# Optimization experiments

Hardware: AMD Instinct MI355X
Metric: run time of the kernel (lower is better)

## Reference

```python
import jax, jax.numpy as jnp
import numpy as np

B, T_ENC, T_DEC = 32, 256, 256
ENC, HID, ATT, CCH, K = 512, 1024, 128, 32, 31
OUT, PRE = 80, 256
ZONEOUT = 0.1
P_DROP = 0.5
PAD = (K - 1) // 2


def setup_inputs() -> dict:
    key = jax.random.key(0)
    ks = jax.random.split(key, 20)
    def n(k, shape, s=0.02):
        return jax.random.normal(k, shape, dtype=jnp.float32) * s
    inp = {}
    inp["encoder_outs"] = jax.random.normal(ks[0], (B, T_ENC, ENC), dtype=jnp.float32)
    inp["decoder_targets"] = jax.random.normal(ks[1], (B, T_DEC, OUT), dtype=jnp.float32)
    keep = 1.0 - P_DROP
    # pre-sampled inverted-dropout masks for the 2 prenet layers at every step
    inp["prenet_masks"] = jax.random.bernoulli(ks[2], keep, (T_DEC, 2, B, PRE)).astype(jnp.float32) / keep
    inp["in_lens"] = jax.random.randint(ks[3], (B,), T_ENC // 2, T_ENC + 1, dtype=jnp.int32)
    # location-sensitive attention params
    inp["V_w"] = n(ks[4], (ATT, ENC)); inp["V_b"] = jnp.zeros((ATT,), jnp.float32)
    inp["W_w"] = n(ks[5], (ATT, HID))
    inp["U_w"] = n(ks[6], (ATT, CCH))
    inp["F_w"] = n(ks[7], (CCH, 1, K))
    inp["w_w"] = n(ks[8], (1, ATT)); inp["w_b"] = jnp.zeros((1,), jnp.float32)
    # prenet
    inp["pre_w0"] = n(ks[9], (PRE, OUT)); inp["pre_b0"] = jnp.zeros((PRE,), jnp.float32)
    inp["pre_w1"] = n(ks[10], (PRE, PRE)); inp["pre_b1"] = jnp.zeros((PRE,), jnp.float32)
    # stacked LSTM cells (zoneout wrappers)
    inp["l0_wih"] = n(ks[11], (4 * HID, ENC + PRE)); inp["l0_whh"] = n(ks[12], (4 * HID, HID))
    inp["l0_bih"] = jnp.zeros((4 * HID,), jnp.float32); inp["l0_bhh"] = jnp.zeros((4 * HID,), jnp.float32)
    inp["l1_wih"] = n(ks[13], (4 * HID, HID)); inp["l1_whh"] = n(ks[14], (4 * HID, HID))
    inp["l1_bih"] = jnp.zeros((4 * HID,), jnp.float32); inp["l1_bhh"] = jnp.zeros((4 * HID,), jnp.float32)
    # output projections
    inp["feat_w"] = n(ks[15], (OUT, ENC + HID))
    inp["prob_w"] = n(ks[16], (1, ENC + HID)); inp["prob_b"] = jnp.zeros((1,), jnp.float32)
    return inp


def _lstm_cell(x, h, c, wih, whh, bih, bhh):
    g = x @ wih.T + bih + h @ whh.T + bhh
    i, f, gg, o = jnp.split(g, 4, axis=1)  # torch LSTMCell gate order
    c2 = jax.nn.sigmoid(f) * c + jax.nn.sigmoid(i) * jnp.tanh(gg)
    h2 = jax.nn.sigmoid(o) * jnp.tanh(c2)
    return h2, c2


def _decode(encoder_outs, decoder_targets, prenet_masks, in_lens,
            V_w, V_b, W_w, U_w, F_w, w_w, w_b,
            pre_w0, pre_b0, pre_w1, pre_b1,
            l0_wih, l0_whh, l0_bih, l0_bhh,
            l1_wih, l1_whh, l1_bih, l1_bhh,
            feat_w, prob_w, prob_b):
    b = encoder_outs.shape[0]
    pad_mask = jnp.arange(T_ENC)[None, :] >= in_lens[:, None]       # [B,T_enc] True = pad
    att_uniform = (~pad_mask).astype(jnp.float32) / in_lens[:, None].astype(jnp.float32)
    processed_memory = encoder_outs @ V_w.T + V_b                   # [B,T_enc,ATT]
    neg = jnp.float32(-1e9)

    # teacher forcing: prev_out at step 0 is the go-frame, then target[t-1]
    targets_prev = jnp.concatenate(
        [jnp.zeros((b, 1, OUT), jnp.float32), decoder_targets[:, :-1]], axis=1)
    xs = (jnp.swapaxes(targets_prev, 0, 1), prenet_masks[:, 0], prenet_masks[:, 1],
          jnp.arange(T_DEC))

    def step(carry, x):
        h0, c0, h1, c1, cum = carry
        prev_out, m0, m1, t = x
        # location-sensitive attention (prev_att_w = None at t=0 -> uniform over valid)
        att_prev = jnp.where(t == 0, att_uniform, cum)              # [B,T_enc]
        f = jax.lax.conv_general_dilated(
            att_prev[:, None, :], F_w, (1,), [(PAD, PAD)],
            dimension_numbers=("NCH", "OIH", "NCH"))                # [B,CCH,T_enc]
        f = jnp.swapaxes(f, 1, 2)                                   # [B,T_enc,CCH]
        erg = jnp.tanh(processed_memory + (h0 @ W_w.T)[:, None, :] + f @ U_w.T)
        erg = (erg @ w_w.T + w_b)[..., 0]                           # [B,T_enc]
        erg = jnp.where(pad_mask, neg, erg)
        aw = jax.nn.softmax(erg, axis=1)
        att_c = jnp.einsum("bt,bte->be", aw, encoder_outs)          # [B,ENC]
        # prenet (dropout always on, via pre-sampled masks)
        p = jax.nn.relu(prev_out @ pre_w0.T + pre_b0) * m0
        p = jax.nn.relu(p @ pre_w1.T + pre_b1) * m1
        xin = jnp.concatenate([att_c, p], axis=1)
        # zoneout LSTM stack (eval-mode zoneout: convex mix of prev/new states)
        h0n, c0n = _lstm_cell(xin, h0, c0, l0_wih, l0_whh, l0_bih, l0_bhh)
        h0 = ZONEOUT * h0 + (1.0 - ZONEOUT) * h0n
        c0 = ZONEOUT * c0 + (1.0 - ZONEOUT) * c0n
        h1n, c1n = _lstm_cell(h0, h1, c1, l1_wih, l1_whh, l1_bih, l1_bhh)
        h1 = ZONEOUT * h1 + (1.0 - ZONEOUT) * h1n
        c1 = ZONEOUT * c1 + (1.0 - ZONEOUT) * c1n
        hcs = jnp.concatenate([h1, att_c], axis=1)                  # [B,HID+ENC]
        out = hcs @ feat_w.T                                        # [B,OUT] (no bias)
        logit = hcs @ prob_w.T + prob_b                             # [B,1]
        return (h0, c0, h1, c1, cum + aw), (out, logit, aw)

    z = jnp.zeros((b, HID), jnp.float32)
    carry0 = (z, z, z, z, jnp.zeros((b, T_ENC), jnp.float32))
    _, (outs, logits, att_ws) = jax.lax.scan(step, carry0, xs)
    outs = jnp.transpose(outs, (1, 2, 0))      # [B,OUT,T_dec]
    logits = logits[..., 0].T                  # [B,T_dec]
    att_ws = jnp.swapaxes(att_ws, 0, 1)        # [B,T_dec,T_enc]
    return outs, logits, att_ws


def reference(encoder_outs, decoder_targets, prenet_masks, in_lens,
              V_w, V_b, W_w, U_w, F_w, w_w, w_b,
              pre_w0, pre_b0, pre_w1, pre_b1,
              l0_wih, l0_whh, l0_bih, l0_bhh,
              l1_wih, l1_whh, l1_bih, l1_bhh,
              feat_w, prob_w, prob_b):
    return _decode(encoder_outs, decoder_targets, prenet_masks, in_lens,
                   V_w, V_b, W_w, U_w, F_w, w_w, w_b,
                   pre_w0, pre_b0, pre_w1, pre_b1,
                   l0_wih, l0_whh, l0_bih, l0_bhh,
                   l1_wih, l1_whh, l1_bih, l1_bhh,
                   feat_w, prob_w, prob_b)
```

## Files before the change

### kernel.cpp

```cpp
#include <hip/hip_runtime.h>

typedef _Float16 half2_t __attribute__((ext_vector_type(2)));
typedef unsigned uint_t;

#define B_    32
#define TE_   256
#define TD_   256
#define ENC_  512
#define HID_  1024
#define ATT_  128
#define OUT_  80
#define PRE_  256

#define LOG_OFF  655360u
#define ATTW_OFF 663552u

#define OFF_PM    0u
#define OFF_P1H   1048576u
#define OFF_M     2097152u
#define OFF_WWHT  2101248u
#define OFF_ENCH  2166784u
#define OFF_W0P   4263936u
#define OFF_W1P   7933952u
#define OFF_XC0   12128256u
#define OFF_XC1   12173312u
#define OFF_C0    12206080u
#define OFF_C1    12238848u
#define OFF_CUM   12271616u
#define OFF_ATTC  12279808u
#define OFF_END   12328960u

__device__ __forceinline__ float rcp_f(float x){ return __builtin_amdgcn_rcpf(x); }
__device__ __forceinline__ float sigm(float x){ return rcp_f(1.0f + __expf(-x)); }
__device__ __forceinline__ float tanh_f(float x){ float e = __expf(2.0f*x); return 1.0f - 2.0f*rcp_f(e+1.0f); }

__device__ __forceinline__ uint_t packh2(float a, float b){
  half2_t h; h[0] = (_Float16)a; h[1] = (_Float16)b;
  return __builtin_bit_cast(uint_t, h);
}
__device__ __forceinline__ float dot2f(uint_t w, uint_t x, float c){
#if __has_builtin(__builtin_amdgcn_fdot2)
  return __builtin_amdgcn_fdot2(__builtin_bit_cast(half2_t, w),
                                __builtin_bit_cast(half2_t, x), c, false);
#else
  half2_t a = __builtin_bit_cast(half2_t, w), b = __builtin_bit_cast(half2_t, x);
  return c + (float)a[0]*(float)b[0] + (float)a[1]*(float)b[1];
#endif
}


__global__ void k_init(float* __restrict__ ws){
  unsigned n = OFF_END - OFF_XC0;
  for (unsigned i = blockIdx.x*blockDim.x + threadIdx.x; i < n; i += gridDim.x*blockDim.x)
    ws[OFF_XC0 + i] = 0.f;
}

__global__ void k_precm(const float* __restrict__ Uw, const float* __restrict__ Fw,
                        float* __restrict__ ws){
  float* M = ws + OFF_M;
  for (int idx = threadIdx.x; idx < 128*31; idx += blockDim.x){
    int a = idx / 31, k = idx % 31;
    float s = 0.f;
    for (int c = 0; c < 32; c++) s += Uw[a*32+c]*Fw[c*31+k];
    M[idx] = s;
  }
}

__global__ void k_cvtww(const float* __restrict__ Ww, float* __restrict__ ws){
  uint_t* WT = (uint_t*)(ws + OFF_WWHT);
  int p = blockIdx.x;
  for (int a = threadIdx.x; a < 128; a += blockDim.x)
    WT[p*128 + a] = packh2(Ww[a*1024 + 2*p], Ww[a*1024 + 2*p + 1]);
}

__global__ void k_packenc(const float* __restrict__ enc, float* __restrict__ ws){
  uint_t* ENCH = (uint_t*)(ws + OFF_ENCH);
  size_t row = blockIdx.x;
  for (int j = threadIdx.x; j < 256; j += blockDim.x)
    ENCH[row*256 + j] = packh2(enc[row*512 + 2*j], enc[row*512 + 2*j + 1]);
}

__global__ void k_packw0(const float* __restrict__ wih, const float* __restrict__ whh,
                         float* __restrict__ ws){
  uint_t* W = (uint_t*)(ws + OFF_W0P);
  size_t r = blockIdx.x;
  for (int p = threadIdx.x; p < 896; p += blockDim.x){
    int k = 2*p;
    const float* src = (k < 768) ? (wih + r*768 + k) : (whh + r*1024 + (k-768));
    W[r*896 + p] = packh2(src[0], src[1]);
  }
}

__global__ void k_packw1(const float* __restrict__ wih, const float* __restrict__ whh,
                         float* __restrict__ ws){
  uint_t* W = (uint_t*)(ws + OFF_W1P);
  size_t r = blockIdx.x;
  for (int p = threadIdx.x; p < 1024; p += blockDim.x){
    int k = 2*p;
    const float* src = (k < 1024) ? (wih + r*1024 + k) : (whh + r*1024 + (k-1024));
    W[r*1024 + p] = packh2(src[0], src[1]);
  }
}

__global__ __launch_bounds__(256) void k_pm(const float* __restrict__ enc,
    const float* __restrict__ Vw, const float* __restrict__ Vb, float* __restrict__ ws){
  float* pm = ws + OFF_PM;
  int b  = blockIdx.x >> 2;
  int s0 = (blockIdx.x & 3) << 6;
  int a  = threadIdx.x & 127;
  int sh = threadIdx.x >> 7;
  __shared__ float Vl[128*65];
  __shared__ float El[64*64];
  float acc[32];
  #pragma unroll
  for (int i=0;i<32;i++) acc[i]=0.f;
  for (int kc=0; kc<ENC_; kc+=64){
    for (int i=threadIdx.x; i<128*64; i+=256){
      int aa = i>>6, kk = i&63;
      Vl[aa*65+kk] = Vw[aa*ENC_ + kc + kk];
    }
    for (int i=threadIdx.x; i<64*64; i+=256){
      int ss = i>>6, kk = i&63;
      El[i] = enc[(size_t)(b*TE_ + s0 + ss)*ENC_ + kc + kk];
    }
    __syncthreads();
    for (int k=0;k<64;k++){
      float va = Vl[a*65+k];
      const float* er = &El[(sh*32)*64 + k];
      #pragma unroll
      for (int s=0;s<32;s++) acc[s] += va * er[s*64];
    }
    __syncthreads();
  }
  float bb = Vb[a];
  for (int s=0;s<32;s++)
    pm[((size_t)b*128 + a)*256 + (s0 + sh*32 + s)] = acc[s] + bb;
}

__global__ __launch_bounds__(256) void k_pre(const float* __restrict__ tgt,
    const float* __restrict__ w0, const float* __restrict__ b0,
    const float* __restrict__ w1, const float* __restrict__ b1,
    const float* __restrict__ masks, float* __restrict__ ws){
  uint_t* P1H = (uint_t*)(ws + OFF_P1H);
  int t = blockIdx.x, j = threadIdx.x;
  __shared__ float xl[32*80];
  __shared__ float p0l[32*256];
  __shared__ float p1s[256*32];
  for (int i=j; i<32*80; i+=256){
    int b = i/80, o = i%80;
    xl[i] = (t==0) ? 0.f : tgt[((size_t)b*TD_ + (t-1))*80 + o];
  }
  __syncthreads();
  {
    float bj = b0[j];
    float w[80];
    #pragma unroll
    for (int o=0;o<80;o++) w[o] = w0[j*80+o];
    for (int b=0;b<32;b++){
      float a0=0,a1=0,a2=0,a3=0;
      const float* x = &xl[b*80];
      #pragma unroll
      for (int o=0;o<80;o+=4){
        a0+=w[o]*x[o]; a1+=w[o+1]*x[o+1]; a2+=w[o+2]*x[o+2]; a3+=w[o+3]*x[o+3];
      }
      float m = masks[(((size_t)t*2+0)*32+b)*256 + j];
      p0l[b*256 + j] = fmaxf(bj+a0+a1+a2+a3, 0.f) * m;
    }
  }
  __syncthreads();
  {
    float bj = b1[j];
    const float4* wr = (const float4*)(w1 + j*256);
    float acc[32];
    #pragma unroll
    for (int i=0;i<32;i++) acc[i]=0.f;
    for (int o4=0;o4<64;o4++){
      float4 w = wr[o4];
      #pragma unroll
      for (int b=0;b<32;b++){
        const float4 xv = *(const float4*)&p0l[b*256 + o4*4];
        acc[b] += w.x*xv.x + w.y*xv.y + w.z*xv.z + w.w*xv.w;
      }
    }
    for (int b=0;b<32;b++){
      float m = masks[(((size_t)t*2+1)*32+b)*256 + j];
      p1s[j*32 + b] = fmaxf(bj+acc[b], 0.f) * m;
    }
  }
  __syncthreads();
  for (int i=j; i<32*128; i+=256){
    int b = i >> 7, jp = i & 127;
    P1H[((size_t)t*32 + b)*128 + jp] = packh2(p1s[(2*jp)*32 + b], p1s[(2*jp+1)*32 + b]);
  }
}


__global__ __launch_bounds__(512) void k_stepa(int t,
    const int* __restrict__ lens, const float* __restrict__ ww, const float* __restrict__ wb,
    const float* __restrict__ featw, const float* __restrict__ probw,
    const float* __restrict__ probb, float* __restrict__ ws, float* __restrict__ out){
  __shared__ __align__(16) uint_t h0l[512];
  __shared__ __align__(16) float Ml[128*32];
  __shared__ __align__(16) float apad[320];
  __shared__ __align__(16) float whl[128];
  __shared__ __align__(16) float wl[128];
  __shared__ __align__(16) float scl[256];
  __shared__ __align__(16) float awl[256];
  __shared__ __align__(16) float redl[128];
  __shared__ __align__(16) float psq[2048];
  __shared__ __align__(16) float redo[512];
  const int blk = blockIdx.x, tid = threadIdx.x;
  const int pc = t & 1, pp = pc ^ 1;
  uint_t* XC0 = (uint_t*)(ws + OFF_XC0);
  uint_t* XC1 = (uint_t*)(ws + OFF_XC1);
  float* ATTC = ws + OFF_ATTC;

  if (blk >= 32){
    if (t < 2) return;
    const int tt = t - 2;
    int ob = blk - 32;
    int b = tid & 31, rr = (tid>>5)&3, ksq = tid>>7;
    int r = ob*4 + rr;
    const float* wr = (r < 80) ? (featw + (size_t)r*1536) : probw;
    const float* acp = ATTC + (size_t)(tt%3)*16384 + b*512;
    float acc = 0.f;
    for (int j=0;j<96;j++){
      int k = ksq*384 + j*4;
      float x0,x1,x2,x3;
      if (k < 1024){
        uint2 hw = *(const uint2*)(XC1 + b*1024 + pc*512 + (k>>1));
        half2_t ha = __builtin_bit_cast(half2_t, hw.x);
        half2_t hb = __builtin_bit_cast(half2_t, hw.y);
        x0 = (float)ha[0]; x1 = (float)ha[1]; x2 = (float)hb[0]; x3 = (float)hb[1];
      } else {
        float4 f = *(const float4*)(acp + (k-1024));
        x0 = f.x; x1 = f.y; x2 = f.z; x3 = f.w;
      }
      if (r <= 80){
        float4 wv = *(const float4*)(wr + k);
        acc += wv.x*x0 + wv.y*x1 + wv.z*x2 + wv.w*x3;
      }
    }
    redo[(rr*4+ksq)*32 + b] = acc;
    __syncthreads();
    if (tid < 128){
      int b2 = tid&31, r2 = tid>>5;
      float vsum = redo[(r2*4+0)*32+b2] + redo[(r2*4+1)*32+b2]
                 + redo[(r2*4+2)*32+b2] + redo[(r2*4+3)*32+b2];
      int rr2 = ob*4 + r2;
      if (rr2 < 80)       out[((size_t)b2*80 + rr2)*256 + tt] = vsum;
      else if (rr2 == 80) out[LOG_OFF + (size_t)b2*256 + tt] = vsum + probb[0];
    }
    return;
  }

  if (t >= TD_) return;
  const int b = blk;
  const int len = lens[b];
  const float* PM = ws + OFF_PM;
  const float* Mg = ws + OFF_M;
  const uint_t* WWHT = (const uint_t*)(ws + OFF_WWHT);
  const uint_t* ENCH = (const uint_t*)(ws + OFF_ENCH);
  const uint_t* P1H = (const uint_t*)(ws + OFF_P1H);
  float* CUM = ws + OFF_CUM;

  if (tid < 128)
    *(uint4*)(h0l + tid*4) = *(const uint4*)(XC0 + b*1408 + 384 + pp*512 + tid*4);
  for (int i=tid; i<128*31; i+=512) Ml[(i/31)*32 + (i%31)] = Mg[i];
  for (int i=tid; i<288; i+=512){
    int p = i - 15;
    float vv = 0.f;
    if (p >= 0 && p < 256)
      vv = (t==0) ? ((p < len) ? 1.0f/(float)len : 0.f) : CUM[b*256 + p];
    apad[i] = vv;
  }
  if (tid < 128) wl[tid] = ww[tid];
  __syncthreads();
  {
    int aW = tid & 127, qW = tid >> 7;
    const uint_t* wt = WWHT + (size_t)(qW*128)*128 + aW;
    const uint_t* hb = h0l + qW*128;
    float s0 = 0.f, s1 = 0.f;
    #pragma unroll 8
    for (int p=0;p<128;p+=2){
      s0 = dot2f(wt[(size_t)p*128],     hb[p],   s0);
      s1 = dot2f(wt[(size_t)(p+1)*128], hb[p+1], s1);
    }
    psq[qW*128 + aW] = s0 + s1;
  }
  __syncthreads();
  if (tid < 128) whl[tid] = psq[tid] + psq[128+tid] + psq[256+tid] + psq[384+tid];
  __syncthreads();
  {
    int pg = tid & 63, q = tid >> 6;
    float apw[36];
    #pragma unroll
    for (int i=0;i<36;i+=4) *(float4*)&apw[i] = *(const float4*)&apad[pg*4 + i];
    float part0=0, part1=0, part2=0, part3=0;
    const float* pmb = PM + (size_t)b*128*256;
    for (int aa=0; aa<16; aa++){
      int a = q*16 + aa;
      const float* mr = Ml + a*32;
      float4 pv = *(const float4*)(pmb + (size_t)a*256 + pg*4);
      float wa = whl[a];
      float u0 = pv.x + wa, u1 = pv.y + wa, u2 = pv.z + wa, u3 = pv.w + wa;
      #pragma unroll
      for (int k=0;k<28;k+=4){
        float4 m4 = *(const float4*)(mr + k);
        u0 += m4.x*apw[k]   + m4.y*apw[k+1] + m4.z*apw[k+2] + m4.w*apw[k+3];
        u1 += m4.x*apw[k+1] + m4.y*apw[k+2] + m4.z*apw[k+3] + m4.w*apw[k+4];
        u2 += m4.x*apw[k+2] + m4.y*apw[k+3] + m4.z*apw[k+4] + m4.w*apw[k+5];
        u3 += m4.x*apw[k+3] + m4.y*apw[k+4] + m4.z*apw[k+5] + m4.w*apw[k+6];
      }
      float m28 = mr[28], m29 = mr[29], m30 = mr[30];
      u0 += m28*apw[28] + m29*apw[29] + m30*apw[30];
      u1 += m28*apw[29] + m29*apw[30] + m30*apw[31];
      u2 += m28*apw[30] + m29*apw[31] + m30*apw[32];
      u3 += m28*apw[31] + m29*apw[32] + m30*apw[33];
      float wv = wl[a];
      part0 += tanh_f(u0)*wv; part1 += tanh_f(u1)*wv;
      part2 += tanh_f(u2)*wv; part3 += tanh_f(u3)*wv;
    }
    float4 pp2; pp2.x = part0; pp2.y = part1; pp2.z = part2; pp2.w = part3;
    *(float4*)&psq[tid*4] = pp2;
  }
  __syncthreads();
  if (tid < 256){
    float s = wb[0];
    int pgg = tid >> 2, d = tid & 3;
    #pragma unroll
    for (int qq=0;qq<8;qq++) s += psq[(qq*64 + pgg)*4 + d];
    scl[tid] = (tid >= len) ? -1.0e9f : s;
  }
  __syncthreads();
  if (tid < 128) redl[tid] = fmaxf(scl[tid], scl[tid+128]);
  __syncthreads();
  if (tid < 64){
    float v = fmaxf(redl[tid], redl[tid+64]);
    #pragma unroll
    for (int off=32; off>0; off>>=1) v = fmaxf(v, __shfl_down(v, off));
    if (tid==0) redl[0] = v;
  }
  __syncthreads();
  float mx = redl[0];
  if (tid < 256) awl[tid] = __expf(scl[tid]-mx);
  __syncthreads();
  if (tid < 128) redl[tid] = awl[tid] + awl[tid+128];
  __syncthreads();
  if (tid < 64){
    float v = redl[tid] + redl[tid+64];
    #pragma unroll
    for (int off=32; off>0; off>>=1) v += __shfl_down(v, off);
    if (tid==0) redl[0] = v;
  }
  __syncthreads();
  float inv = rcp_f(redl[0]);
  if (tid < 256){
    float aw = awl[tid]*inv;
    awl[tid] = aw;
    CUM[b*256 + tid] += aw;
    out[ATTW_OFF + ((size_t)b*TD_ + t)*256 + tid] = aw;
  }
  __syncthreads();
  {
    int el = tid & 127, ph = tid >> 7;
    const uint_t* ep = ENCH + ((size_t)b*256 + ph*64)*256 + el*2;
    float c0=0,c1=0,c2=0,c3=0;
    for (int p=0;p<64;p++){
      float a = awl[ph*64 + p];
      uint2 ev = *(const uint2*)(ep + (size_t)p*256);
      half2_t h0v = __builtin_bit_cast(half2_t, ev.x);
      half2_t h1v = __builtin_bit_cast(half2_t, ev.y);
      c0 += a*(float)h0v[0]; c1 += a*(float)h0v[1];
      c2 += a*(float)h1v[0]; c3 += a*(float)h1v[1];
    }
    float4 ca; ca.x=c0; ca.y=c1; ca.z=c2; ca.w=c3;
    *(float4*)&psq[(ph*128 + el)*4] = ca;
  }
  __syncthreads();
  if (tid < 128){
    float4 s = *(const float4*)&psq[tid*4];
    #pragma unroll
    for (int g=1; g<4; g++){
      float4 o = *(const float4*)&psq[(g*128+tid)*4];
      s.x+=o.x; s.y+=o.y; s.z+=o.z; s.w+=o.w;
    }
    *(float4*)(ATTC + (size_t)(t%3)*16384 + b*512 + tid*4) = s;
    XC0[b*1408 + tid*2]     = packh2(s.x, s.y);
    XC0[b*1408 + tid*2 + 1] = packh2(s.z, s.w);
    XC0[b*1408 + 256 + tid] = P1H[((size_t)t*32 + b)*128 + tid];
  }
}


#define W0S 908
#define W1S 1028
#define LW1 14528u
#define LXB0 30976u
#define LXB1 35200u
#define LTOT 39424u

__global__ __launch_bounds__(512, 1) void k_stepb(int t,
    const float* __restrict__ l0bih, const float* __restrict__ l0bhh,
    const float* __restrict__ l1bih, const float* __restrict__ l1bhh,
    float* __restrict__ ws){
  __shared__ __align__(16) uint_t lds[LTOT];
  uint_t* w0l = lds;
  uint_t* w1l = lds + LW1;
  float*  gs  = (float*)(lds + LW1);
  const int tid = threadIdx.x;
  const int pc = t & 1, pp = pc ^ 1;
  const int bp = tid & 15, ul = (tid>>4)&3, kq = tid>>6;
  const int sb = tid >> 4, sp = (tid & 15)*8;
  const int u0 = blockIdx.x*4;
  uint_t* XC0 = (uint_t*)(ws + OFF_XC0);
  uint_t* XC1 = (uint_t*)(ws + OFF_XC1);
  _Float16* XC0h = (_Float16*)XC0;
  _Float16* XC1h = (_Float16*)XC1;
  float* C0 = ws + OFF_C0;
  float* C1 = ws + OFF_C1;
  const uint_t* W0P = (const uint_t*)(ws + OFF_W0P);
  const uint_t* W1P = (const uint_t*)(ws + OFF_W1P);

  uint4 w0r[7], w1r[8];
  #pragma unroll
  for (int q=0;q<7;q++){
    int i = q*512 + tid;
    int r = i/224, c4 = i - r*224;
    w0r[q] = *(const uint4*)(W0P + (size_t)((r&3)*1024 + u0 + (r>>2))*896 + c4*4);
  }
  #pragma unroll
  for (int q=0;q<8;q++){
    int i = q*512 + tid;
    int r = i>>8, c4 = i&255;
    w1r[q] = *(const uint4*)(W1P + (size_t)((r&3)*1024 + u0 + (r>>2))*1024 + c4*4);
  }
  float b0s[4], b1s[4], c0old=0.f, c1old=0.f, h0old=0.f, h1old=0.f;
  {
    int bb = tid & 31, uu = (tid >> 5) & 3;
    int u = u0 + uu;
    if (tid < 128){
      #pragma unroll
      for (int g=0;g<4;g++){
        b0s[g] = l0bih[g*1024+u] + l0bhh[g*1024+u];
        b1s[g] = l1bih[g*1024+u] + l1bhh[g*1024+u];
      }
      c0old = C0[u*32 + bb];
      c1old = C1[u*32 + bb];
      h0old = (float)XC0h[bb*2816 + 768 + pp*1024 + u];
      h1old = (float)XC1h[bb*2048 + pc*1024 + u];
    }
  }

  float a0[4]={0,0,0,0}, a1[4]={0,0,0,0};

  if (t < TD_){
    uint4 rA0,rA1,rB0,rB1;
    { const uint_t* s = XC0 + sb*1408 + sp;                       rA0=*(const uint4*)s; rA1=*(const uint4*)(s+4); }
    { const uint_t* s = XC0 + sb*1408 + 128 + sp;                 rB0=*(const uint4*)s; rB1=*(const uint4*)(s+4); }
    #pragma unroll
    for (int q=0;q<7;q++){
      int i = q*512 + tid;
      int r = i/224, c4 = i - r*224;
      *(uint4*)(w0l + r*W0S + c4*4) = w0r[q];
    }
    *(uint4*)(lds + LXB0 + sb*132 + sp) = rA0;
    *(uint4*)(lds + LXB0 + sb*132 + sp + 4) = rA1;
    rA0 = rB0; rA1 = rB1;
    { const uint_t* s = XC0 + sb*1408 + 256 + sp;                 rB0=*(const uint4*)s; rB1=*(const uint4*)(s+4); }
    #pragma unroll
    for (int c=0;c<7;c++){
      __syncthreads();
      if (c+1 < 7){
        uint_t* xw = lds + ((c&1) ? LXB0 : LXB1);
        *(uint4*)(xw + sb*132 + sp)     = rA0;
        *(uint4*)(xw + sb*132 + sp + 4) = rA1;
        rA0 = rB0; rA1 = rB1;
        if (c+3 < 7){
          int co = (c+3)*128 + sp;
          const uint_t* s = (co < 384) ? (XC0 + sb*1408 + co)
                                       : (XC0 + sb*1408 + 384 + pp*512 + (co-384));
          rB0 = *(const uint4*)s; rB1 = *(const uint4*)(s+4);
        }
      }
      const uint_t* xr = lds + ((c&1) ? LXB1 : LXB0);
      const uint_t* xpa = xr + bp*132 + kq*16;
      const uint_t* xpb = xr + (bp+16)*132 + kq*16;
      uint4 xa[4], xbv[4];
      #pragma unroll
      for (int j4=0;j4<4;j4++){ xa[j4] = *(const uint4*)(xpa + 4*j4); xbv[j4] = *(const uint4*)(xpb + 4*j4); }
      const int wb_ = c*128 + kq*16;
      #pragma unroll
      for (int g=0; g<4; g++){
        const uint_t* wr = w0l + (g + 4*ul)*W0S + wb_;
        float s0 = a0[g], s1 = a1[g];
        #pragma unroll
        for (int j4=0;j4<4;j4++){
          uint4 w = *(const uint4*)(wr + 4*j4);
          s0 = dot2f(w.x, xa[j4].x, s0); s0 = dot2f(w.y, xa[j4].y, s0);
          s0 = dot2f(w.z, xa[j4].z, s0); s0 = dot2f(w.w, xa[j4].w, s0);
          s1 = dot2f(w.x, xbv[j4].x, s1); s1 = dot2f(w.y, xbv[j4].y, s1);
          s1 = dot2f(w.z, xbv[j4].z, s1); s1 = dot2f(w.w, xbv[j4].w, s1);
        }
        a0[g] = s0; a1[g] = s1;
      }
    }
  }
  uint4 pA0=make_uint4(0,0,0,0), pA1=pA0, pB0=pA0, pB1=pA0;
  if (t >= 1){
    { const uint_t* s = XC0 + sb*1408 + 384 + pp*512 + sp;        pA0=*(const uint4*)s; pA1=*(const uint4*)(s+4); }
    { const uint_t* s = XC0 + sb*1408 + 384 + pp*512 + 128 + sp;  pB0=*(const uint4*)s; pB1=*(const uint4*)(s+4); }
  }
  if (t < TD_){
    __syncthreads();
    #pragma unroll
    for (int g=0; g<4; g++){
      gs[(kq*16 + g + 4*ul)*33 + bp]      = a0[g];
      gs[(kq*16 + g + 4*ul)*33 + bp + 16] = a1[g];
    }
    __syncthreads();
    if (tid < 128){
      int bb = tid & 31, uu = tid >> 5;
      int u = u0 + uu;
      float g4[4];
      #pragma unroll
      for (int g=0; g<4; g++){
        float s = 0.f;
        #pragma unroll
        for (int k2=0;k2<8;k2++) s += gs[(k2*16 + g + 4*uu)*33 + bb];
        g4[g] = s + b0s[g];
      }
      float cn = sigm(g4[1])*c0old + sigm(g4[0])*tanh_f(g4[2]);
      float hn = sigm(g4[3])*tanh_f(cn);
      C0[u*32 + bb] = 0.1f*c0old + 0.9f*cn;
      XC0h[bb*2816 + 768 + pc*1024 + u] = (_Float16)(0.1f*h0old + 0.9f*hn);
    }
  }

  if (t >= 1){
    __syncthreads();
    #pragma unroll
    for (int q=0;q<8;q++){
      int i = q*512 + tid;
      int r = i>>8, c4 = i&255;
      *(uint4*)(w1l + r*W1S + c4*4) = w1r[q];
    }
    *(uint4*)(lds + LXB0 + sb*132 + sp)     = pA0;
    *(uint4*)(lds + LXB0 + sb*132 + sp + 4) = pA1;
    pA0 = pB0; pA1 = pB1;
    { const uint_t* s = XC0 + sb*1408 + 384 + pp*512 + 256 + sp;  pB0=*(const uint4*)s; pB1=*(const uint4*)(s+4); }
    float e0[4]={0,0,0,0}, e1[4]={0,0,0,0};
    #pragma unroll
    for (int c=0;c<8;c++){
      __syncthreads();
      if (c+1 < 8){
        uint_t* xw = lds + ((c&1) ? LXB0 : LXB1);
        *(uint4*)(xw + sb*132 + sp)     = pA0;
        *(uint4*)(xw + sb*132 + sp + 4) = pA1;
        pA0 = pB0; pA1 = pB1;
        if (c+3 < 8){
          int co = (c+3)*128 + sp;
          const uint_t* s = (co < 512) ? (XC0 + sb*1408 + 384 + pp*512 + co)
                                       : (XC1 + sb*1024 + pc*512 + (co-512));
          pB0 = *(const uint4*)s; pB1 = *(const uint4*)(s+4);
        }
      }
      const uint_t* xr = lds + ((c&1) ? LXB1 : LXB0);
      const uint_t* xpa = xr + bp*132 + kq*16;
      const uint_t* xpb = xr + (bp+16)*132 + kq*16;
      uint4 xa[4], xbv[4];
      #pragma unroll
      for (int j4=0;j4<4;j4++){ xa[j4] = *(const uint4*)(xpa + 4*j4); xbv[j4] = *(const uint4*)(xpb + 4*j4); }
      const int wb_ = c*128 + kq*16;
      #pragma unroll
      for (int g=0; g<4; g++){
        const uint_t* wr = w1l + (g + 4*ul)*W1S + wb_;
        float s0 = e0[g], s1 = e1[g];
        #pragma unroll
        for (int j4=0;j4<4;j4++){
          uint4 w = *(const uint4*)(wr + 4*j4);
          s0 = dot2f(w.x, xa[j4].x, s0); s0 = dot2f(w.y, xa[j4].y, s0);
          s0 = dot2f(w.z, xa[j4].z, s0); s0 = dot2f(w.w, xa[j4].w, s0);
          s1 = dot2f(w.x, xbv[j4].x, s1); s1 = dot2f(w.y, xbv[j4].y, s1);
          s1 = dot2f(w.z, xbv[j4].z, s1); s1 = dot2f(w.w, xbv[j4].w, s1);
        }
        e0[g] = s0; e1[g] = s1;
      }
    }
    __syncthreads();
    #pragma unroll
    for (int g=0; g<4; g++){
      gs[(kq*16 + g + 4*ul)*33 + bp]      = e0[g];
      gs[(kq*16 + g + 4*ul)*33 + bp + 16] = e1[g];
    }
    __syncthreads();
    if (tid < 128){
      int bb = tid & 31, uu = tid >> 5;
      int u = u0 + uu;
      float g4[4];
      #pragma unroll
      for (int g=0; g<4; g++){
        float s = 0.f;
        #pragma unroll
        for (int k2=0;k2<8;k2++) s += gs[(k2*16 + g + 4*uu)*33 + bb];
        g4[g] = s + b1s[g];
      }
      float cn = sigm(g4[1])*c1old + sigm(g4[0])*tanh_f(g4[2]);
      float hn = sigm(g4[3])*tanh_f(cn);
      C1[u*32 + bb] = 0.1f*c1old + 0.9f*cn;
      XC1h[bb*2048 + pp*1024 + u] = (_Float16)(0.1f*h1old + 0.9f*hn);
    }
  }
}

extern "C" void kernel_launch(void* const* d_in, const int* in_sizes, int n_in,
                              void* d_out, int out_size, void* d_ws, size_t ws_size,
                              hipStream_t stream){
  const float* enc   = (const float*)d_in[0];
  const float* tgt   = (const float*)d_in[1];
  const float* masks = (const float*)d_in[2];
  const int*   lens  = (const int*)  d_in[3];
  const float* Vw    = (const float*)d_in[4];
  const float* Vb    = (const float*)d_in[5];
  const float* Ww    = (const float*)d_in[6];
  const float* Uw    = (const float*)d_in[7];
  const float* Fw    = (const float*)d_in[8];
  const float* ww    = (const float*)d_in[9];
  const float* wb    = (const float*)d_in[10];
  const float* pw0   = (const float*)d_in[11];
  const float* pb0   = (const float*)d_in[12];
  const float* pw1   = (const float*)d_in[13];
  const float* pb1   = (const float*)d_in[14];
  const float* l0wih = (const float*)d_in[15];
  const float* l0whh = (const float*)d_in[16];
  const float* l0bih = (const float*)d_in[17];
  const float* l0bhh = (const float*)d_in[18];
  const float* l1wih = (const float*)d_in[19];
  const float* l1whh = (const float*)d_in[20];
  const float* l1bih = (const float*)d_in[21];
  const float* l1bhh = (const float*)d_in[22];
  const float* featw = (const float*)d_in[23];
  const float* probw = (const float*)d_in[24];
  const float* probb = (const float*)d_in[25];
  float* ws  = (float*)d_ws;
  float* out = (float*)d_out;

  k_init   <<<256, 256,0,stream>>>(ws);
  k_pre    <<<256, 256,0,stream>>>(tgt, pw0, pb0, pw1, pb1, masks, ws);
  k_precm  <<<1,   256,0,stream>>>(Uw, Fw, ws);
  k_cvtww  <<<512, 128,0,stream>>>(Ww, ws);
  k_packenc<<<8192,256,0,stream>>>(enc, ws);
  k_packw0 <<<4096,256,0,stream>>>(l0wih, l0whh, ws);
  k_packw1 <<<4096,256,0,stream>>>(l1wih, l1whh, ws);
  k_pm     <<<128, 256,0,stream>>>(enc, Vw, Vb, ws);

  for (int t = 0; t < TD_; t++){
    k_stepa<<<56, 512,0,stream>>>(t, lens, ww, wb, featw, probw, probb, ws, out);
    k_stepb<<<256,512,0,stream>>>(t, l0bih, l0bhh, l1bih, l1bhh, ws);
  }
  k_stepb<<<256,512,0,stream>>>(256, l0bih, l0bhh, l1bih, l1bhh, ws);
  k_stepa<<<56, 512,0,stream>>>(256, lens, ww, wb, featw, probw, probb, ws, out);
  k_stepa<<<56, 512,0,stream>>>(257, lens, ww, wb, featw, probw, probb, ws, out);
}
```

Before: 16.49 ms.

## Fuse per-step kernels into one persistent cooperative kernel with grid sync

Replaces the 2×256 per-timestep launches of k_stepa and k_stepb with a single cooperative persistent kernel that loops over timesteps and uses grid.sync between steps. LSTM weight slices are loaded into LDS once and stay resident, where before they were reloaded through registers every launch. This is meant to remove launch overhead and the repeated weight reloads. In exchange the attention and LSTM phases now run in the same LDS space on shared blocks, so the phases can no longer overlap across kernels, and every step pays a grid-wide barrier.

Measured after the change: 28.68 ms. +73.9%, slower.

```diff
diff --git a/kernel.cpp b/kernel.cpp
--- a/kernel.cpp
+++ b/kernel.cpp
@@ -1,4 +1,7 @@
 #include <hip/hip_runtime.h>
+#include <hip/hip_cooperative_groups.h>
+
+namespace cg = cooperative_groups;
 
 typedef _Float16 half2_t __attribute__((ext_vector_type(2)));
 typedef unsigned uint_t;
@@ -195,421 +198,408 @@
 }
 
 
-__global__ __launch_bounds__(512) void k_stepa(int t,
+#define W0S 904
+#define W1S 1028
+#define LW1  14464u
+#define LXD  30912u
+#define LXB1 35136u
+#define LTOT 39360u
+
+__global__ __launch_bounds__(512, 2) void k_main(
     const int* __restrict__ lens, const float* __restrict__ ww, const float* __restrict__ wb,
     const float* __restrict__ featw, const float* __restrict__ probw,
-    const float* __restrict__ probb, float* __restrict__ ws, float* __restrict__ out){
-  __shared__ __align__(16) uint_t h0l[512];
-  __shared__ __align__(16) float Ml[128*32];
-  __shared__ __align__(16) float apad[320];
-  __shared__ __align__(16) float whl[128];
-  __shared__ __align__(16) float wl[128];
-  __shared__ __align__(16) float scl[256];
-  __shared__ __align__(16) float awl[256];
-  __shared__ __align__(16) float redl[128];
-  __shared__ __align__(16) float psq[2048];
-  __shared__ __align__(16) float redo[512];
-  const int blk = blockIdx.x, tid = threadIdx.x;
-  const int pc = t & 1, pp = pc ^ 1;
-  uint_t* XC0 = (uint_t*)(ws + OFF_XC0);
-  uint_t* XC1 = (uint_t*)(ws + OFF_XC1);
-  float* ATTC = ws + OFF_ATTC;
-
-  if (blk >= 32){
-    if (t < 2) return;
-    const int tt = t - 2;
-    int ob = blk - 32;
-    int b = tid & 31, rr = (tid>>5)&3, ksq = tid>>7;
-    int r = ob*4 + rr;
-    const float* wr = (r < 80) ? (featw + (size_t)r*1536) : probw;
-    const float* acp = ATTC + (size_t)(tt%3)*16384 + b*512;
-    float acc = 0.f;
-    for (int j=0;j<96;j++){
-      int k = ksq*384 + j*4;
-      float x0,x1,x2,x3;
-      if (k < 1024){
-        uint2 hw = *(const uint2*)(XC1 + b*1024 + pc*512 + (k>>1));
-        half2_t ha = __builtin_bit_cast(half2_t, hw.x);
-        half2_t hb = __builtin_bit_cast(half2_t, hw.y);
-        x0 = (float)ha[0]; x1 = (float)ha[1]; x2 = (float)hb[0]; x3 = (float)hb[1];
-      } else {
-        float4 f = *(const float4*)(acp + (k-1024));
-        x0 = f.x; x1 = f.y; x2 = f.z; x3 = f.w;
-      }
-      if (r <= 80){
-        float4 wv = *(const float4*)(wr + k);
-        acc += wv.x*x0 + wv.y*x1 + wv.z*x2 + wv.w*x3;
-      }
-    }
-    redo[(rr*4+ksq)*32 + b] = acc;
-    __syncthreads();
-    if (tid < 128){
-      int b2 = tid&31, r2 = tid>>5;
-      float vsum = redo[(r2*4+0)*32+b2] + redo[(r2*4+1)*32+b2]
-                 + redo[(r2*4+2)*32+b2] + redo[(r2*4+3)*32+b2];
-      int rr2 = ob*4 + r2;
-      if (rr2 < 80)       out[((size_t)b2*80 + rr2)*256 + tt] = vsum;
-      else if (rr2 == 80) out[LOG_OFF + (size_t)b2*256 + tt] = vsum + probb[0];
-    }
-    return;
-  }
-
-  if (t >= TD_) return;
-  const int b = blk;
-  const int len = lens[b];
-  const float* PM = ws + OFF_PM;
-  const float* Mg = ws + OFF_M;
-  const uint_t* WWHT = (const uint_t*)(ws + OFF_WWHT);
-  const uint_t* ENCH = (const uint_t*)(ws + OFF_ENCH);
-  const uint_t* P1H = (const uint_t*)(ws + OFF_P1H);
-  float* CUM = ws + OFF_CUM;
-
-  if (tid < 128)
-    *(uint4*)(h0l + tid*4) = *(const uint4*)(XC0 + b*1408 + 384 + pp*512 + tid*4);
-  for (int i=tid; i<128*31; i+=512) Ml[(i/31)*32 + (i%31)] = Mg[i];
-  for (int i=tid; i<288; i+=512){
-    int p = i - 15;
-    float vv = 0.f;
-    if (p >= 0 && p < 256)
-      vv = (t==0) ? ((p < len) ? 1.0f/(float)len : 0.f) : CUM[b*256 + p];
-    apad[i] = vv;
-  }
-  if (tid < 128) wl[tid] = ww[tid];
-  __syncthreads();
-  {
-    int aW = tid & 127, qW = tid >> 7;
-    const uint_t* wt = WWHT + (size_t)(qW*128)*128 + aW;
-    const uint_t* hb = h0l + qW*128;
-    float s0 = 0.f, s1 = 0.f;
-    #pragma unroll 8
-    for (int p=0;p<128;p+=2){
-      s0 = dot2f(wt[(size_t)p*128],     hb[p],   s0);
-      s1 = dot2f(wt[(size_t)(p+1)*128], hb[p+1], s1);
-    }
-    psq[qW*128 + aW] = s0 + s1;
-  }
-  __syncthreads();
-  if (tid < 128) whl[tid] = psq[tid] + psq[128+tid] + psq[256+tid] + psq[384+tid];
-  __syncthreads();
-  {
-    int pg = tid & 63, q = tid >> 6;
-    float apw[36];
-    #pragma unroll
-    for (int i=0;i<36;i+=4) *(float4*)&apw[i] = *(const float4*)&apad[pg*4 + i];
-    float part0=0, part1=0, part2=0, part3=0;
-    const float* pmb = PM + (size_t)b*128*256;
-    for (int aa=0; aa<16; aa++){
-      int a = q*16 + aa;
-      const float* mr = Ml + a*32;
-      float4 pv = *(const float4*)(pmb + (size_t)a*256 + pg*4);
-      float wa = whl[a];
-      float u0 = pv.x + wa, u1 = pv.y + wa, u2 = pv.z + wa, u3 = pv.w + wa;
-      #pragma unroll
-      for (int k=0;k<28;k+=4){
-        float4 m4 = *(const float4*)(mr + k);
-        u0 += m4.x*apw[k]   + m4.y*apw[k+1] + m4.z*apw[k+2] + m4.w*apw[k+3];
-        u1 += m4.x*apw[k+1] + m4.y*apw[k+2] + m4.z*apw[k+3] + m4.w*apw[k+4];
-        u2 += m4.x*apw[k+2] + m4.y*apw[k+3] + m4.z*apw[k+4] + m4.w*apw[k+5];
-        u3 += m4.x*apw[k+3] + m4.y*apw[k+4] + m4.z*apw[k+5] + m4.w*apw[k+6];
-      }
-      float m28 = mr[28], m29 = mr[29], m30 = mr[30];
-      u0 += m28*apw[28] + m29*apw[29] + m30*apw[30];
-      u1 += m28*apw[29] + m29*apw[30] + m30*apw[31];
-      u2 += m28*apw[30] + m29*apw[31] + m30*apw[32];
-      u3 += m28*apw[31] + m29*apw[32] + m30*apw[33];
-      float wv = wl[a];
-      part0 += tanh_f(u0)*wv; part1 += tanh_f(u1)*wv;
-      part2 += tanh_f(u2)*wv; part3 += tanh_f(u3)*wv;
-    }
-    float4 pp2; pp2.x = part0; pp2.y = part1; pp2.z = part2; pp2.w = part3;
-    *(float4*)&psq[tid*4] = pp2;
-  }
-  __syncthreads();
-  if (tid < 256){
-    float s = wb[0];
-    int pgg = tid >> 2, d = tid & 3;
-    #pragma unroll
-    for (int qq=0;qq<8;qq++) s += psq[(qq*64 + pgg)*4 + d];
-    scl[tid] = (tid >= len) ? -1.0e9f : s;
-  }
-  __syncthreads();
-  if (tid < 128) redl[tid] = fmaxf(scl[tid], scl[tid+128]);
-  __syncthreads();
-  if (tid < 64){
-    float v = fmaxf(redl[tid], redl[tid+64]);
-    #pragma unroll
-    for (int off=32; off>0; off>>=1) v = fmaxf(v, __shfl_down(v, off));
-    if (tid==0) redl[0] = v;
-  }
-  __syncthreads();
-  float mx = redl[0];
-  if (tid < 256) awl[tid] = __expf(scl[tid]-mx);
-  __syncthreads();
-  if (tid < 128) redl[tid] = awl[tid] + awl[tid+128];
-  __syncthreads();
-  if (tid < 64){
-    float v = redl[tid] + redl[tid+64];
-    #pragma unroll
-    for (int off=32; off>0; off>>=1) v += __shfl_down(v, off);
-    if (tid==0) redl[0] = v;
-  }
-  __syncthreads();
-  float inv = rcp_f(redl[0]);
-  if (tid < 256){
-    float aw = awl[tid]*inv;
-    awl[tid] = aw;
-    CUM[b*256 + tid] += aw;
-    out[ATTW_OFF + ((size_t)b*TD_ + t)*256 + tid] = aw;
-  }
-  __syncthreads();
-  {
-    int el = tid & 127, ph = tid >> 7;
-    const uint_t* ep = ENCH + ((size_t)b*256 + ph*64)*256 + el*2;
-    float c0=0,c1=0,c2=0,c3=0;
-    for (int p=0;p<64;p++){
-      float a = awl[ph*64 + p];
-      uint2 ev = *(const uint2*)(ep + (size_t)p*256);
-      half2_t h0v = __builtin_bit_cast(half2_t, ev.x);
-      half2_t h1v = __builtin_bit_cast(half2_t, ev.y);
-      c0 += a*(float)h0v[0]; c1 += a*(float)h0v[1];
-      c2 += a*(float)h1v[0]; c3 += a*(float)h1v[1];
-    }
-    float4 ca; ca.x=c0; ca.y=c1; ca.z=c2; ca.w=c3;
-    *(float4*)&psq[(ph*128 + el)*4] = ca;
-  }
-  __syncthreads();
-  if (tid < 128){
-    float4 s = *(const float4*)&psq[tid*4];
-    #pragma unroll
-    for (int g=1; g<4; g++){
-      float4 o = *(const float4*)&psq[(g*128+tid)*4];
-      s.x+=o.x; s.y+=o.y; s.z+=o.z; s.w+=o.w;
-    }
-    *(float4*)(ATTC + (size_t)(t%3)*16384 + b*512 + tid*4) = s;
-    XC0[b*1408 + tid*2]     = packh2(s.x, s.y);
-    XC0[b*1408 + tid*2 + 1] = packh2(s.z, s.w);
-    XC0[b*1408 + 256 + tid] = P1H[((size_t)t*32 + b)*128 + tid];
-  }
-}
-
-
-#define W0S 908
-#define W1S 1028
-#define LW1 14528u
-#define LXB0 30976u
-#define LXB1 35200u
-#define LTOT 39424u
-
-__global__ __launch_bounds__(512, 1) void k_stepb(int t,
+    const float* __restrict__ probb,
     const float* __restrict__ l0bih, const float* __restrict__ l0bhh,
     const float* __restrict__ l1bih, const float* __restrict__ l1bhh,
-    float* __restrict__ ws){
+    float* __restrict__ ws, float* __restrict__ out)
+{
   __shared__ __align__(16) uint_t lds[LTOT];
+  cg::grid_group grid = cg::this_grid();
+
   uint_t* w0l = lds;
   uint_t* w1l = lds + LW1;
-  float*  gs  = (float*)(lds + LW1);
-  const int tid = threadIdx.x;
-  const int pc = t & 1, pp = pc ^ 1;
+  uint_t* xd  = lds + LXD;
+  float*  gs  = (float*)xd;
+  uint_t* h0l = xd;
+  float* Ml   = (float*)(xd + 512);
+  float* apad = (float*)(xd + 4608);
+  float* whl  = (float*)(xd + 4928);
+  float* wl   = (float*)(xd + 5056);
+  float* scl  = (float*)(xd + 5184);
+  float* awl  = (float*)(xd + 5440);
+  float* redl = (float*)(xd + 5696);
+  float* psq  = (float*)(xd + 5824);
+  float* redo = (float*)xd;
+
+  const int blk = blockIdx.x, tid = threadIdx.x;
   const int bp = tid & 15, ul = (tid>>4)&3, kq = tid>>6;
   const int sb = tid >> 4, sp = (tid & 15)*8;
-  const int u0 = blockIdx.x*4;
+  const int u0 = blk*4;
+
   uint_t* XC0 = (uint_t*)(ws + OFF_XC0);
   uint_t* XC1 = (uint_t*)(ws + OFF_XC1);
   _Float16* XC0h = (_Float16*)XC0;
   _Float16* XC1h = (_Float16*)XC1;
   float* C0 = ws + OFF_C0;
   float* C1 = ws + OFF_C1;
-  const uint_t* W0P = (const uint_t*)(ws + OFF_W0P);
-  const uint_t* W1P = (const uint_t*)(ws + OFF_W1P);
-
-  uint4 w0r[7], w1r[8];
-  #pragma unroll
-  for (int q=0;q<7;q++){
-    int i = q*512 + tid;
-    int r = i/224, c4 = i - r*224;
-    w0r[q] = *(const uint4*)(W0P + (size_t)((r&3)*1024 + u0 + (r>>2))*896 + c4*4);
-  }
-  #pragma unroll
-  for (int q=0;q<8;q++){
-    int i = q*512 + tid;
-    int r = i>>8, c4 = i&255;
-    w1r[q] = *(const uint4*)(W1P + (size_t)((r&3)*1024 + u0 + (r>>2))*1024 + c4*4);
-  }
-  float b0s[4], b1s[4], c0old=0.f, c1old=0.f, h0old=0.f, h1old=0.f;
+  float* CUM = ws + OFF_CUM;
+  float* ATTC = ws + OFF_ATTC;
+  const float* PM = ws + OFF_PM;
+  const float* Mg = ws + OFF_M;
+  const uint_t* WWHT = (const uint_t*)(ws + OFF_WWHT);
+  const uint_t* ENCH = (const uint_t*)(ws + OFF_ENCH);
+  const uint_t* P1H  = (const uint_t*)(ws + OFF_P1H);
+
   {
-    int bb = tid & 31, uu = (tid >> 5) & 3;
+    const uint_t* W0P = (const uint_t*)(ws + OFF_W0P);
+    const uint_t* W1P = (const uint_t*)(ws + OFF_W1P);
+    for (int i=tid; i<16*224; i+=512){
+      int r = i/224, c4 = i - r*224;
+      *(uint4*)(w0l + r*W0S + c4*4) =
+        *(const uint4*)(W0P + (size_t)((r&3)*1024 + u0 + (r>>2))*896 + c4*4);
+    }
+    for (int i=tid; i<16*256; i+=512){
+      int r = i>>8, c4 = i&255;
+      *(uint4*)(w1l + r*W1S + c4*4) =
+        *(const uint4*)(W1P + (size_t)((r&3)*1024 + u0 + (r>>2))*1024 + c4*4);
+    }
+  }
+  float b0s[4]={0,0,0,0}, b1s[4]={0,0,0,0};
+  if (tid < 128){
+    int uu = tid >> 5;
     int u = u0 + uu;
-    if (tid < 128){
-      #pragma unroll
-      for (int g=0;g<4;g++){
-        b0s[g] = l0bih[g*1024+u] + l0bhh[g*1024+u];
-        b1s[g] = l1bih[g*1024+u] + l1bhh[g*1024+u];
-      }
-      c0old = C0[u*32 + bb];
-      c1old = C1[u*32 + bb];
-      h0old = (float)XC0h[bb*2816 + 768 + pp*1024 + u];
-      h1old = (float)XC1h[bb*2048 + pc*1024 + u];
-    }
-  }
-
-  float a0[4]={0,0,0,0}, a1[4]={0,0,0,0};
-
-  if (t < TD_){
-    uint4 rA0,rA1,rB0,rB1;
-    { const uint_t* s = XC0 + sb*1408 + sp;                       rA0=*(const uint4*)s; rA1=*(const uint4*)(s+4); }
-    { const uint_t* s = XC0 + sb*1408 + 128 + sp;                 rB0=*(const uint4*)s; rB1=*(const uint4*)(s+4); }
     #pragma unroll
-    for (int q=0;q<7;q++){
-      int i = q*512 + tid;
-      int r = i/224, c4 = i - r*224;
-      *(uint4*)(w0l + r*W0S + c4*4) = w0r[q];
-    }
-    *(uint4*)(lds + LXB0 + sb*132 + sp) = rA0;
-    *(uint4*)(lds + LXB0 + sb*132 + sp + 4) = rA1;
-    rA0 = rB0; rA1 = rB1;
-    { const uint_t* s = XC0 + sb*1408 + 256 + sp;                 rB0=*(const uint4*)s; rB1=*(const uint4*)(s+4); }
-    #pragma unroll
-    for (int c=0;c<7;c++){
+    for (int g=0;g<4;g++){
+      b0s[g] = l0bih[g*1024+u] + l0bhh[g*1024+u];
+      b1s[g] = l1bih[g*1024+u] + l1bhh[g*1024+u];
+    }
+  }
+  __syncthreads();
+
+  for (int t = 0; t < 258; ++t){
+    const int pc = t & 1, pp = pc ^ 1;
+
+    if (blk < 32){
+      if (t < TD_){
+        const int b = blk;
+        const int len = lens[b];
+        if (tid < 128)
+          *(uint4*)(h0l + tid*4) = *(const uint4*)(XC0 + b*1408 + 384 + pp*512 + tid*4);
+        for (int i=tid; i<128*31; i+=512) Ml[(i/31)*32 + (i%31)] = Mg[i];
+        for (int i=tid; i<288; i+=512){
+          int p = i - 15;
+          float vv = 0.f;
+          if (p >= 0 && p < 256)
+            vv = (t==0) ? ((p < len) ? 1.0f/(float)len : 0.f) : CUM[b*256 + p];
+          apad[i] = vv;
+        }
+        if (tid < 128) wl[tid] = ww[tid];
+        __syncthreads();
+        {
+          int aW = tid & 127, qW = tid >> 7;
+          const uint_t* wt = WWHT + (size_t)(qW*128)*128 + aW;
+          const uint_t* hb = h0l + qW*128;
+          float s0 = 0.f, s1 = 0.f;
+          #pragma unroll 8
+          for (int p=0;p<128;p+=2){
+            s0 = dot2f(wt[(size_t)p*128],     hb[p],   s0);
+            s1 = dot2f(wt[(size_t)(p+1)*128], hb[p+1], s1);
+          }
+          psq[qW*128 + aW] = s0 + s1;
+        }
+        __syncthreads();
+        if (tid < 128) whl[tid] = psq[tid] + psq[128+tid] + psq[256+tid] + psq[384+tid];
+        __syncthreads();
+        {
+          int pg = tid & 63, q = tid >> 6;
+          float apw[36];
+          #pragma unroll
+          for (int i=0;i<36;i+=4) *(float4*)&apw[i] = *(const float4*)&apad[pg*4 + i];
+          float part0=0, part1=0, part2=0, part3=0;
+          const float* pmb = PM + (size_t)b*128*256;
+          for (int aa=0; aa<16; aa++){
+            int a = q*16 + aa;
+            const float* mr = Ml + a*32;
+            float4 pv = *(const float4*)(pmb + (size_t)a*256 + pg*4);
+            float wa = whl[a];
+            float u0_ = pv.x + wa, u1_ = pv.y + wa, u2_ = pv.z + wa, u3_ = pv.w + wa;
+            #pragma unroll
+            for (int k=0;k<28;k+=4){
+              float4 m4 = *(const float4*)(mr + k);
+              u0_ += m4.x*apw[k]   + m4.y*apw[k+1] + m4.z*apw[k+2] + m4.w*apw[k+3];
+              u1_ += m4.x*apw[k+1] + m4.y*apw[k+2] + m4.z*apw[k+3] + m4.w*apw[k+4];
+              u2_ += m4.x*apw[k+2] + m4.y*apw[k+3] + m4.z*apw[k+4] + m4.w*apw[k+5];
+              u3_ += m4.x*apw[k+3] + m4.y*apw[k+4] + m4.z*apw[k+5] + m4.w*apw[k+6];
+            }
+            float m28 = mr[28], m29 = mr[29], m30 = mr[30];
+            u0_ += m28*apw[28] + m29*apw[29] + m30*apw[30];
+            u1_ += m28*apw[29] + m29*apw[30] + m30*apw[31];
+            u2_ += m28*apw[30] + m29*apw[31] + m30*apw[32];
+            u3_ += m28*apw[31] + m29*apw[32] + m30*apw[33];
+            float wv = wl[a];
+            part0 += tanh_f(u0_)*wv; part1 += tanh_f(u1_)*wv;
+            part2 += tanh_f(u2_)*wv; part3 += tanh_f(u3_)*wv;
+          }
+          float4 pq; pq.x = part0; pq.y = part1; pq.z = part2; pq.w = part3;
+          *(float4*)&psq[tid*4] = pq;
+        }
+        __syncthreads();
+        if (tid < 256){
+          float s = wb[0];
+          int pgg = tid >> 2, d = tid & 3;
+          #pragma unroll
+          for (int qq=0;qq<8;qq++) s += psq[(qq*64 + pgg)*4 + d];
+          scl[tid] = (tid >= len) ? -1.0e9f : s;
+        }
+        __syncthreads();
+        if (tid < 128) redl[tid] = fmaxf(scl[tid], scl[tid+128]);
+        __syncthreads();
+        if (tid < 64){
+          float v = fmaxf(redl[tid], redl[tid+64]);
+          #pragma unroll
+          for (int off=32; off>0; off>>=1) v = fmaxf(v, __shfl_down(v, off));
+          if (tid==0) redl[0] = v;
+        }
+        __syncthreads();
+        float mx = redl[0];
+        if (tid < 256) awl[tid] = __expf(scl[tid]-mx);
+        __syncthreads();
+        if (tid < 128) redl[tid] = awl[tid] + awl[tid+128];
+        __syncthreads();
+        if (tid < 64){
+          float v = redl[tid] + redl[tid+64];
+          #pragma unroll
+          for (int off=32; off>0; off>>=1) v += __shfl_down(v, off);
+          if (tid==0) redl[0] = v;
+        }
+        __syncthreads();
+        float inv = rcp_f(redl[0]);
+        if (tid < 256){
+          float aw = awl[tid]*inv;
+          awl[tid] = aw;
+          CUM[b*256 + tid] += aw;
+          out[ATTW_OFF + ((size_t)b*TD_ + t)*256 + tid] = aw;
+        }
+        __syncthreads();
+        {
+          int el = tid & 127, ph = tid >> 7;
+          const uint_t* ep = ENCH + ((size_t)b*256 + ph*64)*256 + el*2;
+          float c0=0,c1=0,c2=0,c3=0;
+          for (int p=0;p<64;p++){
+            float a = awl[ph*64 + p];
+            uint2 ev = *(const uint2*)(ep + (size_t)p*256);
+            half2_t h0v = __builtin_bit_cast(half2_t, ev.x);
+            half2_t h1v = __builtin_bit_cast(half2_t, ev.y);
+            c0 += a*(float)h0v[0]; c1 += a*(float)h0v[1];
+            c2 += a*(float)h1v[0]; c3 += a*(float)h1v[1];
+          }
+          float4 ca; ca.x=c0; ca.y=c1; ca.z=c2; ca.w=c3;
+          *(float4*)&psq[(ph*128 + el)*4] = ca;
+        }
+        __syncthreads();
+        if (tid < 128){
+          float4 s = *(const float4*)&psq[tid*4];
+          #pragma unroll
+          for (int g=1; g<4; g++){
+            float4 o = *(const float4*)&psq[(g*128+tid)*4];
+            s.x+=o.x; s.y+=o.y; s.z+=o.z; s.w+=o.w;
+          }
+          *(float4*)(ATTC + (size_t)(t%3)*16384 + b*512 + tid*4) = s;
+          XC0[b*1408 + tid*2]     = packh2(s.x, s.y);
+          XC0[b*1408 + tid*2 + 1] = packh2(s.z, s.w);
+          XC0[b*1408 + 256 + tid] = P1H[((size_t)t*32 + b)*128 + tid];
+        }
+      }
+    } else if (blk < 56){
+      if (t >= 2){
+        const int tt = t - 2;
+        int ob = blk - 32;
+        int b = tid & 31, rr = (tid>>5)&3, ksq = tid>>7;
+        int r = ob*4 + rr;
+        const float* wr = (r < 80) ? (featw + (size_t)r*1536) : probw;
+        const float* acp = ATTC + (size_t)(tt%3)*16384 + b*512;
+        float acc = 0.f;
+        for (int j=0;j<96;j++){
+          int k = ksq*384 + j*4;
+          float x0,x1,x2,x3;
+          if (k < 1024){
+            uint2 hw = *(const uint2*)(XC1 + b*1024 + pc*512 + (k>>1));
+            half2_t ha = __builtin_bit_cast(half2_t, hw.x);
+            half2_t hb = __builtin_bit_cast(half2_t, hw.y);
+            x0 = (float)ha[0]; x1 = (float)ha[1]; x2 = (float)hb[0]; x3 = (float)hb[1];
+          } else {
+            float4 f = *(const float4*)(acp + (k-1024));
+            x0 = f.x; x1 = f.y; x2 = f.z; x3 = f.w;
+          }
+          if (r <= 80){
+            float4 wv = *(const float4*)(wr + k);
+            acc += wv.x*x0 + wv.y*x1 + wv.z*x2 + wv.w*x3;
+          }
+        }
+        redo[(rr*4+ksq)*32 + b] = acc;
+        __syncthreads();
+        if (tid < 128){
+          int b2 = tid&31, r2 = tid>>5;
+          float vsum = redo[(r2*4+0)*32+b2] + redo[(r2*4+1)*32+b2]
+                     + redo[(r2*4+2)*32+b2] + redo[(r2*4+3)*32+b2];
+          int rr2 = ob*4 + r2;
+          if (rr2 < 80)       out[((size_t)b2*80 + rr2)*256 + tt] = vsum;
+          else if (rr2 == 80) out[LOG_OFF + (size_t)b2*256 + tt] = vsum + probb[0];
+        }
+      }
+    }
+    grid.sync();
+
+    float a0[4]={0,0,0,0}, a1[4]={0,0,0,0};
+    if (t < TD_){
+      uint4 rA0,rA1,rB0,rB1;
+      { const uint_t* s = XC0 + sb*1408 + sp;        rA0=*(const uint4*)s; rA1=*(const uint4*)(s+4); }
+      { const uint_t* s = XC0 + sb*1408 + 128 + sp;  rB0=*(const uint4*)s; rB1=*(const uint4*)(s+4); }
+      *(uint4*)(xd + sb*132 + sp)     = rA0;
+      *(uint4*)(xd + sb*132 + sp + 4) = rA1;
+      rA0 = rB0; rA1 = rB1;
+      { const uint_t* s = XC0 + sb*1408 + 256 + sp;  rB0=*(const uint4*)s; rB1=*(const uint4*)(s+4); }
+      #pragma unroll 1
+      for (int c=0;c<7;c++){
+        __syncthreads();
+        if (c+1 < 7){
+          uint_t* xw = lds + ((c&1) ? LXD : LXB1);
+          *(uint4*)(xw + sb*132 + sp)     = rA0;
+          *(uint4*)(xw + sb*132 + sp + 4) = rA1;
+          rA0 = rB0; rA1 = rB1;
+          if (c+3 < 7){
+            int co = (c+3)*128 + sp;
+            const uint_t* s = (co < 384) ? (XC0 + sb*1408 + co)
+                                         : (XC0 + sb*1408 + 384 + pp*512 + (co-384));
+            rB0 = *(const uint4*)s; rB1 = *(const uint4*)(s+4);
+          }
+        }
+        const uint_t* xr = lds + ((c&1) ? LXB1 : LXD);
+        const uint_t* xpa = xr + bp*132 + kq*16;
+        const uint_t* xpb = xr + (bp+16)*132 + kq*16;
+        uint4 xa[4], xbv[4];
+        #pragma unroll
+        for (int j4=0;j4<4;j4++){ xa[j4] = *(const uint4*)(xpa + 4*j4); xbv[j4] = *(const uint4*)(xpb + 4*j4); }
+        const int wb_ = c*128 + kq*16;
+        #pragma unroll
+        for (int g=0; g<4; g++){
+          const uint_t* wr = w0l + (g + 4*ul)*W0S + wb_;
+          float s0 = a0[g], s1 = a1[g];
+          #pragma unroll
+          for (int j4=0;j4<4;j4++){
+            uint4 w = *(const uint4*)(wr + 4*j4);
+            s0 = dot2f(w.x, xa[j4].x, s0); s0 = dot2f(w.y, xa[j4].y, s0);
+            s0 = dot2f(w.z, xa[j4].z, s0); s0 = dot2f(w.w, xa[j4].w, s0);
+            s1 = dot2f(w.x, xbv[j4].x, s1); s1 = dot2f(w.y, xbv[j4].y, s1);
+            s1 = dot2f(w.z, xbv[j4].z, s1); s1 = dot2f(w.w, xbv[j4].w, s1);
+          }
+          a0[g] = s0; a1[g] = s1;
+        }
+      }
+    }
+    uint4 pA0=make_uint4(0,0,0,0), pA1=pA0, pB0=pA0, pB1=pA0;
+    if (t >= 1 && t <= 256){
+      { const uint_t* s = XC0 + sb*1408 + 384 + pp*512 + sp;        pA0=*(const uint4*)s; pA1=*(const uint4*)(s+4); }
+      { const uint_t* s = XC0 + sb*1408 + 384 + pp*512 + 128 + sp;  pB0=*(const uint4*)s; pB1=*(const uint4*)(s+4); }
+    }
+    if (t < TD_){
       __syncthreads();
-      if (c+1 < 7){
-        uint_t* xw = lds + ((c&1) ? LXB0 : LXB1);
-        *(uint4*)(xw + sb*132 + sp)     = rA0;
-        *(uint4*)(xw + sb*132 + sp + 4) = rA1;
-        rA0 = rB0; rA1 = rB1;
-        if (c+3 < 7){
-          int co = (c+3)*128 + sp;
-          const uint_t* s = (co < 384) ? (XC0 + sb*1408 + co)
-                                       : (XC0 + sb*1408 + 384 + pp*512 + (co-384));
-          rB0 = *(const uint4*)s; rB1 = *(const uint4*)(s+4);
-        }
-      }
-      const uint_t* xr = lds + ((c&1) ? LXB1 : LXB0);
-      const uint_t* xpa = xr + bp*132 + kq*16;
-      const uint_t* xpb = xr + (bp+16)*132 + kq*16;
-      uint4 xa[4], xbv[4];
-      #pragma unroll
-      for (int j4=0;j4<4;j4++){ xa[j4] = *(const uint4*)(xpa + 4*j4); xbv[j4] = *(const uint4*)(xpb + 4*j4); }
-      const int wb_ = c*128 + kq*16;
       #pragma unroll
       for (int g=0; g<4; g++){
-        const uint_t* wr = w0l + (g + 4*ul)*W0S + wb_;
-        float s0 = a0[g], s1 = a1[g];
+        gs[(kq*16 + g + 4*ul)*33 + bp]      = a0[g];
+        gs[(kq*16 + g + 4*ul)*33 + bp + 16] = a1[g];
+      }
+      __syncthreads();
+      if (tid < 128){
+        int bb = tid & 31, uu = tid >> 5;
+        int u = u0 + uu;
+        float g4[4];
         #pragma unroll
-        for (int j4=0;j4<4;j4++){
-          uint4 w = *(const uint4*)(wr + 4*j4);
-          s0 = dot2f(w.x, xa[j4].x, s0); s0 = dot2f(w.y, xa[j4].y, s0);
-          s0 = dot2f(w.z, xa[j4].z, s0); s0 = dot2f(w.w, xa[j4].w, s0);
-          s1 = dot2f(w.x, xbv[j4].x, s1); s1 = dot2f(w.y, xbv[j4].y, s1);
-          s1 = dot2f(w.z, xbv[j4].z, s1); s1 = dot2f(w.w, xbv[j4].w, s1);
-        }
-        a0[g] = s0; a1[g] = s1;
-      }
-    }
-  }
-  uint4 pA0=make_uint4(0,0,0,0), pA1=pA0, pB0=pA0, pB1=pA0;
-  if (t >= 1){
-    { const uint_t* s = XC0 + sb*1408 + 384 + pp*512 + sp;        pA0=*(const uint4*)s; pA1=*(const uint4*)(s+4); }
-    { const uint_t* s = XC0 + sb*1408 + 384 + pp*512 + 128 + sp;  pB0=*(const uint4*)s; pB1=*(const uint4*)(s+4); }
-  }
-  if (t < TD_){
-    __syncthreads();
-    #pragma unroll
-    for (int g=0; g<4; g++){
-      gs[(kq*16 + g + 4*ul)*33 + bp]      = a0[g];
-      gs[(kq*16 + g + 4*ul)*33 + bp + 16] = a1[g];
-    }
-    __syncthreads();
-    if (tid < 128){
-      int bb = tid & 31, uu = tid >> 5;
-      int u = u0 + uu;
-      float g4[4];
+        for (int g=0; g<4; g++){
+          float s = 0.f;
+          #pragma unroll
+          for (int k2=0;k2<8;k2++) s += gs[(k2*16 + g + 4*uu)*33 + bb];
+          g4[g] = s + b0s[g];
+        }
+        float c_old = C0[u*32 + bb];
+        float h_old = (float)XC0h[bb*2816 + 768 + pp*1024 + u];
+        float cn = sigm(g4[1])*c_old + sigm(g4[0])*tanh_f(g4[2]);
+        float hn = sigm(g4[3])*tanh_f(cn);
+        C0[u*32 + bb] = 0.1f*c_old + 0.9f*cn;
+        XC0h[bb*2816 + 768 + pc*1024 + u] = (_Float16)(0.1f*h_old + 0.9f*hn);
+      }
+    }
+    if (t >= 1 && t <= 256){
+      __syncthreads();
+      *(uint4*)(xd + sb*132 + sp)     = pA0;
+      *(uint4*)(xd + sb*132 + sp + 4) = pA1;
+      pA0 = pB0; pA1 = pB1;
+      { const uint_t* s = XC0 + sb*1408 + 384 + pp*512 + 256 + sp;  pB0=*(const uint4*)s; pB1=*(const uint4*)(s+4); }
+      float e0[4]={0,0,0,0}, e1[4]={0,0,0,0};
+      #pragma unroll 1
+      for (int c=0;c<8;c++){
+        __syncthreads();
+        if (c+1 < 8){
+          uint_t* xw = lds + ((c&1) ? LXD : LXB1);
+          *(uint4*)(xw + sb*132 + sp)     = pA0;
+          *(uint4*)(xw + sb*132 + sp + 4) = pA1;
+          pA0 = pB0; pA1 = pB1;
+          if (c+3 < 8){
+            int co = (c+3)*128 + sp;
+            const uint_t* s = (co < 512) ? (XC0 + sb*1408 + 384 + pp*512 + co)
+                                         : (XC1 + sb*1024 + pc*512 + (co-512));
+            pB0 = *(const uint4*)s; pB1 = *(const uint4*)(s+4);
+          }
+        }
+        const uint_t* xr = lds + ((c&1) ? LXB1 : LXD);
+        const uint_t* xpa = xr + bp*132 + kq*16;
+        const uint_t* xpb = xr + (bp+16)*132 + kq*16;
+        uint4 xa[4], xbv[4];
+        #pragma unroll
+        for (int j4=0;j4<4;j4++){ xa[j4] = *(const uint4*)(xpa + 4*j4); xbv[j4] = *(const uint4*)(xpb + 4*j4); }
+        const int wb_ = c*128 + kq*16;
+        #pragma unroll
+        for (int g=0; g<4; g++){
+          const uint_t* wr = w1l + (g + 4*ul)*W1S + wb_;
+          float s0 = e0[g], s1 = e1[g];
+          #pragma unroll
+          for (int j4=0;j4<4;j4++){
+            uint4 w = *(const uint4*)(wr + 4*j4);
+            s0 = dot2f(w.x, xa[j4].x, s0); s0 = dot2f(w.y, xa[j4].y, s0);
+            s0 = dot2f(w.z, xa[j4].z, s0); s0 = dot2f(w.w, xa[j4].w, s0);
+            s1 = dot2f(w.x, xbv[j4].x, s1); s1 = dot2f(w.y, xbv[j4].y, s1);
+            s1 = dot2f(w.z, xbv[j4].z, s1); s1 = dot2f(w.w, xbv[j4].w, s1);
+          }
+          e0[g] = s0; e1[g] = s1;
+        }
+      }
+      __syncthreads();
       #pragma unroll
       for (int g=0; g<4; g++){
-        float s = 0.f;
+        gs[(kq*16 + g + 4*ul)*33 + bp]      = e0[g];
+        gs[(kq*16 + g + 4*ul)*33 + bp + 16] = e1[g];
+      }
+      __syncthreads();
+      if (tid < 128){
+        int bb = tid & 31, uu = tid >> 5;
+        int u = u0 + uu;
+        float g4[4];
         #pragma unroll
-        for (int k2=0;k2<8;k2++) s += gs[(k2*16 + g + 4*uu)*33 + bb];
-        g4[g] = s + b0s[g];
-      }
-      float cn = sigm(g4[1])*c0old + sigm(g4[0])*tanh_f(g4[2]);
-      float hn = sigm(g4[3])*tanh_f(cn);
-      C0[u*32 + bb] = 0.1f*c0old + 0.9f*cn;
-      XC0h[bb*2816 + 768 + pc*1024 + u] = (_Float16)(0.1f*h0old + 0.9f*hn);
-    }
-  }
-
-  if (t >= 1){
-    __syncthreads();
-    #pragma unroll
-    for (int q=0;q<8;q++){
-      int i = q*512 + tid;
-      int r = i>>8, c4 = i&255;
-      *(uint4*)(w1l + r*W1S + c4*4) = w1r[q];
-    }
-    *(uint4*)(lds + LXB0 + sb*132 + sp)     = pA0;
-    *(uint4*)(lds + LXB0 + sb*132 + sp + 4) = pA1;
-    pA0 = pB0; pA1 = pB1;
-    { const uint_t* s = XC0 + sb*1408 + 384 + pp*512 + 256 + sp;  pB0=*(const uint4*)s; pB1=*(const uint4*)(s+4); }
-    float e0[4]={0,0,0,0}, e1[4]={0,0,0,0};
-    #pragma unroll
-    for (int c=0;c<8;c++){
-      __syncthreads();
-      if (c+1 < 8){
-        uint_t* xw = lds + ((c&1) ? LXB0 : LXB1);
-        *(uint4*)(xw + sb*132 + sp)     = pA0;
-        *(uint4*)(xw + sb*132 + sp + 4) = pA1;
-        pA0 = pB0; pA1 = pB1;
-        if (c+3 < 8){
-          int co = (c+3)*128 + sp;
-          const uint_t* s = (co < 512) ? (XC0 + sb*1408 + 384 + pp*512 + co)
-                                       : (XC1 + sb*1024 + pc*512 + (co-512));
-          pB0 = *(const uint4*)s; pB1 = *(const uint4*)(s+4);
-        }
-      }
-      const uint_t* xr = lds + ((c&1) ? LXB1 : LXB0);
-      const uint_t* xpa = xr + bp*132 + kq*16;
-      const uint_t* xpb = xr + (bp+16)*132 + kq*16;
-      uint4 xa[4], xbv[4];
-      #pragma unroll
-      for (int j4=0;j4<4;j4++){ xa[j4] = *(const uint4*)(xpa + 4*j4); xbv[j4] = *(const uint4*)(xpb + 4*j4); }
-      const int wb_ = c*128 + kq*16;
-      #pragma unroll
-      for (int g=0; g<4; g++){
-        const uint_t* wr = w1l + (g + 4*ul)*W1S + wb_;
-        float s0 = e0[g], s1 = e1[g];
-        #pragma unroll
-        for (int j4=0;j4<4;j4++){
-          uint4 w = *(const uint4*)(wr + 4*j4);
-          s0 = dot2f(w.x, xa[j4].x, s0); s0 = dot2f(w.y, xa[j4].y, s0);
-          s0 = dot2f(w.z, xa[j4].z, s0); s0 = dot2f(w.w, xa[j4].w, s0);
-          s1 = dot2f(w.x, xbv[j4].x, s1); s1 = dot2f(w.y, xbv[j4].y, s1);
-          s1 = dot2f(w.z, xbv[j4].z, s1); s1 = dot2f(w.w, xbv[j4].w, s1);
-        }
-        e0[g] = s0; e1[g] = s1;
-      }
-    }
-    __syncthreads();
-    #pragma unroll
-    for (int g=0; g<4; g++){
-      gs[(kq*16 + g + 4*ul)*33 + bp]      = e0[g];
-      gs[(kq*16 + g + 4*ul)*33 + bp + 16] = e1[g];
-    }
-    __syncthreads();
-    if (tid < 128){
-      int bb = tid & 31, uu = tid >> 5;
-      int u = u0 + uu;
-      float g4[4];
-      #pragma unroll
-      for (int g=0; g<4; g++){
-        float s = 0.f;
-        #pragma unroll
-        for (int k2=0;k2<8;k2++) s += gs[(k2*16 + g + 4*uu)*33 + bb];
-        g4[g] = s + b1s[g];
-      }
-      float cn = sigm(g4[1])*c1old + sigm(g4[0])*tanh_f(g4[2]);
-      float hn = sigm(g4[3])*tanh_f(cn);
-      C1[u*32 + bb] = 0.1f*c1old + 0.9f*cn;
-      XC1h[bb*2048 + pp*1024 + u] = (_Float16)(0.1f*h1old + 0.9f*hn);
-    }
+        for (int g=0; g<4; g++){
+          float s = 0.f;
+          #pragma unroll
+          for (int k2=0;k2<8;k2++) s += gs[(k2*16 + g + 4*uu)*33 + bb];
+          g4[g] = s + b1s[g];
+        }
+        float c_old = C1[u*32 + bb];
+        float h_old = (float)XC1h[bb*2048 + pc*1024 + u];
+        float cn = sigm(g4[1])*c_old + sigm(g4[0])*tanh_f(g4[2]);
+        float hn = sigm(g4[3])*tanh_f(cn);
+        C1[u*32 + bb] = 0.1f*c_old + 0.9f*cn;
+        XC1h[bb*2048 + pp*1024 + u] = (_Float16)(0.1f*h_old + 0.9f*hn);
+      }
+    }
+    grid.sync();
   }
 }
 
@@ -654,11 +644,11 @@
   k_packw1 <<<4096,256,0,stream>>>(l1wih, l1whh, ws);
   k_pm     <<<128, 256,0,stream>>>(enc, Vw, Vb, ws);
 
-  for (int t = 0; t < TD_; t++){
-    k_stepa<<<56, 512,0,stream>>>(t, lens, ww, wb, featw, probw, probb, ws, out);
-    k_stepb<<<256,512,0,stream>>>(t, l0bih, l0bhh, l1bih, l1bhh, ws);
-  }
-  k_stepb<<<256,512,0,stream>>>(256, l0bih, l0bhh, l1bih, l1bhh, ws);
-  k_stepa<<<56, 512,0,stream>>>(256, lens, ww, wb, featw, probw, probb, ws, out);
-  k_stepa<<<56, 512,0,stream>>>(257, lens, ww, wb, featw, probw, probb, ws, out);
-}
+  void* args[] = {
+    (void*)&lens, (void*)&ww, (void*)&wb,
+    (void*)&featw, (void*)&probw, (void*)&probb,
+    (void*)&l0bih, (void*)&l0bhh, (void*)&l1bih, (void*)&l1bhh,
+    (void*)&ws, (void*)&out
+  };
+  hipLaunchCooperativeKernel((void*)k_main, dim3(256), dim3(512), args, 0, stream);
+}
```
